# Kernel tuning notes

Measured on AMD Instinct MI355X. Metric: run time of the kernel, lower is better.

Reference implementation:

```python
import jax, jax.numpy as jnp
import numpy as np

N = 20000      # nodes
E = 640000     # edges
FIN = 128
FQK = 128
FV = 128
H = 8
FH = FQK // H   # 16
FHV = FV // H   # 16
FTOT = 2 * FQK + FV


def setup_inputs() -> dict:
    key = jax.random.key(0)
    kx, kw, ks, kd, kb = jax.random.split(key, 5)
    x = jax.random.normal(kx, (N, FIN), dtype=jnp.float32)
    # nn.Linear(Fin, Ftot, bias=False): weight [Ftot, Fin]
    W = jax.random.normal(kw, (FTOT, FIN), dtype=jnp.float32) / np.sqrt(FIN)
    # src must be sorted (scatter ops assume grouped-by-src, size src[-1]+1)
    src = jnp.sort(jax.random.randint(ks, (E,), 0, N, dtype=jnp.int64))
    src = src.at[-1].set(N - 1)  # ensure full output size N
    dest = jax.random.randint(kd, (E,), 0, N, dtype=jnp.int64)
    ei = jnp.stack([src, dest])
    batch = jnp.sort(jax.random.randint(kb, (N,), 0, 16, dtype=jnp.int64))
    return {"x": x, "W": W, "batch": batch, "ei": ei}


def reference(x, W, batch, ei):
    src, dest = ei[0], ei[1]
    scaling = float(FH) ** (-0.5)
    proj = x @ W.T                                  # [N, Ftot]
    q, k, v = jnp.split(proj, [FQK, 2 * FQK], axis=-1)
    q = (q * scaling).reshape(-1, H, FH)            # [N, H, Fh]
    k = k.reshape(-1, H, FH)
    v = v.reshape(-1, H, FHV)
    qs, ks, vs = q[src], k[dest], v[dest]           # [E, H, Fh] gathers
    aw = jnp.einsum('ehf,ehf->eh', qs, ks)          # per-edge dot products
    # scatter_softmax: global (not per-segment) max subtraction, as in source
    xm = aw.max(axis=0)                              # [H]
    exp = jnp.exp(aw - xm) + 1e-8                    # [E, H]
    expsum = jax.ops.segment_sum(exp, src, num_segments=N)[src]
    attn = exp / expsum                              # [E, H]
    out = jax.ops.segment_sum(attn[:, :, None] * vs, src, num_segments=N)
    return out.reshape(-1, H * FHV)                  # [N, Fv]
```

## Files before the change

kernel.cpp:

```cpp
#include <hip/hip_runtime.h>

constexpr int FIN = 128;

constexpr float XM0 = 8.0f;

typedef __attribute__((ext_vector_type(8))) short bf8x;
typedef __attribute__((ext_vector_type(4))) float f4x;
typedef _Float16 h2 __attribute__((ext_vector_type(2)));

__device__ inline unsigned short f2bf(float v) {
  unsigned int u = __float_as_uint(v);
  unsigned int r = u + 0x7FFFu + ((u >> 16) & 1u);
  return (unsigned short)(r >> 16);
}
__device__ inline float bf2f(unsigned short s) {
  return __uint_as_float(((unsigned int)s) << 16);
}
__device__ inline unsigned short f2h(float v) {
  _Float16 h = (_Float16)v;
  return __builtin_bit_cast(unsigned short, h);
}
__device__ inline h2 bch2(float f) { return __builtin_bit_cast(h2, f); }
__device__ inline float bcf(h2 h) { return __builtin_bit_cast(float, h); }

__device__ inline float dot2acc(h2 a, h2 b, float c) {
#if __has_builtin(__builtin_amdgcn_fdot2)
  return __builtin_amdgcn_fdot2(a, b, c, false);
#else
  return c + (float)a[0] * (float)b[0] + (float)a[1] * (float)b[1];
#endif
}

__global__ __launch_bounds__(256, 2) void proj_kernel(
    const float* __restrict__ x, const float* __restrict__ W,
    unsigned short* __restrict__ qg, unsigned short* __restrict__ kvg, int N,
    const int* __restrict__ src, const int* __restrict__ dest,
    unsigned short* __restrict__ dest16, int* __restrict__ row_ptr, int E) {
  __shared__ unsigned short xhi[128][72], xlo[128][72];
  __shared__ unsigned short whi[128][72], wlo[128][72];

  const int tid = threadIdx.x;
  const int r0 = blockIdx.y * 128;
  const int c0 = blockIdx.x * 128;

  {
    const int gid = (blockIdx.y * gridDim.x + blockIdx.x) * 256 + tid;
    const int tot = gridDim.x * gridDim.y * 256;
    for (int i = gid; i < E; i += tot) dest16[i] = (unsigned short)dest[i];
    if (gid <= N) {
      int lo = 0, hi = E;
      while (lo < hi) {
        int mid = (lo + hi) >> 1;
        if (src[mid] < gid) lo = mid + 1; else hi = mid;
      }
      row_ptr[gid] = lo;
    }
  }

  const int lane = tid & 63;
  const int w = tid >> 6;
  const int mbase = (w >> 1) * 64;
  const int nbase = (w & 1) * 64;
  const int lr = lane & 15;
  const int q4 = lane >> 4;

  f4x acc[4][4];
#pragma unroll
  for (int mt = 0; mt < 4; ++mt)
#pragma unroll
    for (int nt = 0; nt < 4; ++nt)
#pragma unroll
      for (int k = 0; k < 4; ++k) acc[mt][nt][k] = 0.f;

  for (int p = 0; p < 2; ++p) {
    if (p) __syncthreads();
#pragma unroll
    for (int pass = 0; pass < 8; ++pass) {
      const int idx = tid + pass * 256;
      const int kq = idx & 15, r = idx >> 4;
      float4 xv = make_float4(0.f, 0.f, 0.f, 0.f);
      if (r0 + r < N) xv = *(const float4*)(x + (size_t)(r0 + r) * FIN + p * 64 + kq * 4);
      const float4 wv = *(const float4*)(W + (size_t)(c0 + r) * FIN + p * 64 + kq * 4);
      const float xa[4] = {xv.x, xv.y, xv.z, xv.w};
      const float wa[4] = {wv.x, wv.y, wv.z, wv.w};
      unsigned short xh[4], xl[4], wh[4], wl[4];
#pragma unroll
      for (int i = 0; i < 4; ++i) {
        xh[i] = f2bf(xa[i]); xl[i] = f2bf(xa[i] - bf2f(xh[i]));
        wh[i] = f2bf(wa[i]); wl[i] = f2bf(wa[i] - bf2f(wh[i]));
      }
      *(ushort4*)&xhi[r][kq * 4] = make_ushort4(xh[0], xh[1], xh[2], xh[3]);
      *(ushort4*)&xlo[r][kq * 4] = make_ushort4(xl[0], xl[1], xl[2], xl[3]);
      *(ushort4*)&whi[r][kq * 4] = make_ushort4(wh[0], wh[1], wh[2], wh[3]);
      *(ushort4*)&wlo[r][kq * 4] = make_ushort4(wl[0], wl[1], wl[2], wl[3]);
    }
    __syncthreads();

#pragma unroll
    for (int kit = 0; kit < 2; ++kit) {
      const int ko = kit * 32 + q4 * 8;
      bf8x ah[4], al[4], bh[4], bl[4];
#pragma unroll
      for (int i2 = 0; i2 < 4; ++i2) {
        ah[i2] = *(const bf8x*)&xhi[mbase + i2 * 16 + lr][ko];
        al[i2] = *(const bf8x*)&xlo[mbase + i2 * 16 + lr][ko];
        bh[i2] = *(const bf8x*)&whi[nbase + i2 * 16 + lr][ko];
        bl[i2] = *(const bf8x*)&wlo[nbase + i2 * 16 + lr][ko];
      }
#pragma unroll
      for (int mt = 0; mt < 4; ++mt)
#pragma unroll
        for (int nt = 0; nt < 4; ++nt) {
          acc[mt][nt] = __builtin_amdgcn_mfma_f32_16x16x32_bf16(ah[mt], bh[nt], acc[mt][nt], 0, 0, 0);
          acc[mt][nt] = __builtin_amdgcn_mfma_f32_16x16x32_bf16(ah[mt], bl[nt], acc[mt][nt], 0, 0, 0);
          acc[mt][nt] = __builtin_amdgcn_mfma_f32_16x16x32_bf16(al[mt], bh[nt], acc[mt][nt], 0, 0, 0);
        }
    }
  }

#pragma unroll
  for (int mt = 0; mt < 4; ++mt)
#pragma unroll
    for (int nt = 0; nt < 4; ++nt)
#pragma unroll
      for (int rr = 0; rr < 4; ++rr) {
        const int row = r0 + mbase + mt * 16 + q4 * 4 + rr;
        if (row < N) {
          const int c = c0 + nbase + nt * 16 + lr;
          const float v = acc[mt][nt][rr];
          if (c < 128) {
            const int head = c >> 4, g = head >> 2, hg = head & 3;
            const int seg = hg * 2 + ((c >> 3) & 1), feat = c & 7;
            qg[((size_t)g * N + row) * 64 + seg * 8 + feat] = f2h(v * 0.25f);
          } else if (c < 256) {
            const int cc = c - 128;
            const int head = cc >> 4, g = head >> 2, hg = head & 3;
            const int seg = hg * 2 + ((cc >> 3) & 1), feat = cc & 7;
            kvg[((size_t)g * N + row) * 128 + seg * 8 + feat] = f2h(v);
          } else {
            const int cc = c - 256;
            const int head = cc >> 4, g = head >> 2, hg = head & 3;
            const int seg = hg * 2 + ((cc >> 3) & 1), feat = cc & 7;
            kvg[((size_t)g * N + row) * 128 + 64 + seg * 8 + feat] = f2h(v);
          }
        }
      }
}

__global__ __launch_bounds__(256, 8) void attn_kernel(
    const unsigned short* __restrict__ qg_, const unsigned short* __restrict__ kvg_,
    const unsigned short* __restrict__ dest16, const int* __restrict__ row_ptr,
    float* __restrict__ out, int N) {
  const _Float16* qg = (const _Float16*)qg_;
  const _Float16* kvg = (const _Float16*)kvg_;

  const int lane = threadIdx.x & 63;
  const int wid = __builtin_amdgcn_readfirstlane(threadIdx.x >> 6);
  const int g = blockIdx.x & 1;
  const int n = (blockIdx.x >> 1) * 4 + wid;
  if (n >= N) return;

  const int seg = lane & 7;
  const int slot = lane >> 3;

  const int e0 = row_ptr[n], e1 = row_ptr[n + 1];

  h2 q2[4];
  {
    const float4 qv = *(const float4*)(qg + ((size_t)g * N + n) * 64 + seg * 8);
    q2[0] = bch2(qv.x); q2[1] = bch2(qv.y); q2[2] = bch2(qv.z); q2[3] = bch2(qv.w);
  }

  const _Float16* kvb = kvg + (size_t)g * N * 128;
  h2 acc4[4] = {h2{0, 0}, h2{0, 0}, h2{0, 0}, h2{0, 0}};
  float es = 0.f;

  for (int cb = e0; cb < e1; cb += 64) {
    const int ee = cb + lane;
    const int dv = dest16[(ee < e1) ? ee : (e1 - 1)];

    const int rem = e1 - cb;
    const int nch = (rem < 64) ? ((rem + 7) >> 3) : 8;

    auto ldkv = [&](int j, float4& kk, float4& vv) {
      const int sl = j * 8 + slot;
      const int d = __shfl(dv, sl);
      const _Float16* kp = kvb + (size_t)d * 128 + seg * 8;
      kk = *(const float4*)kp;
      vv = *(const float4*)(kp + 64);
    };

    auto comp = [&](int j, const float4& kk, const float4& vv) {
      float p = 0.f;
      p = dot2acc(q2[0], bch2(kk.x), p);
      p = dot2acc(q2[1], bch2(kk.y), p);
      p = dot2acc(q2[2], bch2(kk.z), p);
      p = dot2acc(q2[3], bch2(kk.w), p);
      const float s = p + __shfl_xor(p, 1);
      const int e = cb + j * 8 + slot;
      const float a = (e < e1) ? (__expf(s - XM0) + 1e-8f) : 0.f;
      es += a;
      const _Float16 a1 = (_Float16)a;
      const h2 av = {a1, a1};
      acc4[0] = __builtin_elementwise_fma(av, bch2(vv.x), acc4[0]);
      acc4[1] = __builtin_elementwise_fma(av, bch2(vv.y), acc4[1]);
      acc4[2] = __builtin_elementwise_fma(av, bch2(vv.z), acc4[2]);
      acc4[3] = __builtin_elementwise_fma(av, bch2(vv.w), acc4[3]);
    };

    float4 kkA, vvA, kkB, vvB;
    ldkv(0, kkA, vvA);
    ldkv(1, kkB, vvB);

    for (int j = 0; j < nch; j += 2) {
      float4 kkA2, vvA2, kkB2, vvB2;
      const bool pf = (j + 2 < nch);
      if (pf) { ldkv(j + 2, kkA2, vvA2); ldkv(j + 3, kkB2, vvB2); }
      comp(j, kkA, vvA);
      comp(j + 1, kkB, vvB);
      if (pf) { kkA = kkA2; vvA = vvA2; kkB = kkB2; vvB = vvB2; }
    }
  }

#pragma unroll
  for (int st = 8; st <= 32; st <<= 1) {
#pragma unroll
    for (int j = 0; j < 4; ++j) {
      const h2 o = bch2(__shfl_xor(bcf(acc4[j]), st));
      acc4[j] = acc4[j] + o;
    }
    es += __shfl_xor(es, st);
  }

  if (slot == 0) {
    const float inv = (e1 > e0) ? (1.0f / es) : 0.f;
    const int head = g * 4 + (seg >> 1);
    const int half = seg & 1;
    float o[8];
#pragma unroll
    for (int j = 0; j < 4; ++j) {
      o[2 * j] = (float)acc4[j][0] * inv;
      o[2 * j + 1] = (float)acc4[j][1] * inv;
    }
    float* op = out + (size_t)n * 128 + head * 16 + half * 8;
    *(float4*)op = make_float4(o[0], o[1], o[2], o[3]);
    *(float4*)(op + 4) = make_float4(o[4], o[5], o[6], o[7]);
  }
}

extern "C" void kernel_launch(void* const* d_in, const int* in_sizes, int n_in,
                              void* d_out, int out_size, void* d_ws, size_t ws_size,
                              hipStream_t stream) {
  const float* x = (const float*)d_in[0];
  const float* W = (const float*)d_in[1];
  const int* ei = (const int*)d_in[3];

  const int N = in_sizes[0] / FIN;
  const int E = in_sizes[3] / 2;
  const int* src = ei;
  const int* dst = ei + E;
  float* out = (float*)d_out;

  char* ws = (char*)d_ws;
  unsigned short* qg = (unsigned short*)ws;
  size_t off = (size_t)2 * N * 64 * sizeof(unsigned short);
  unsigned short* kvg = (unsigned short*)(ws + off);
  off += (size_t)2 * N * 128 * sizeof(unsigned short);
  unsigned short* dest16 = (unsigned short*)(ws + off);
  off += ((size_t)E * sizeof(unsigned short) + 15) & ~15ull;
  int* row_ptr = (int*)(ws + off);

  dim3 pgrid(3, (N + 127) / 128);
  proj_kernel<<<pgrid, 256, 0, stream>>>(x, W, qg, kvg, N, src, dst, dest16, row_ptr, E);
  attn_kernel<<<((N + 3) / 4) * 2, 256, 0, stream>>>(qg, kvg, dest16, row_ptr, out, N);
}
```

Baseline: 115.7 us.

## Process two nodes per wavefront by splitting lanes into half-wave groups

The attention kernel now gives each 64-lane wavefront two destination nodes, one per 32-lane half, with 4 edge slots per half instead of 8 for one node. Edge chunks shrink to 32, and the loop runs while either half still has edges. The cross-slot reduction drops one shuffle stage and the grid is halved. The goal is to cut per-wave fixed overhead and reduction cost on low-degree nodes. The cost is that each wave now loops until the busier of its two nodes is done, so imbalance between paired nodes wastes lanes.

```diff
diff --git a/kernel.cpp b/kernel.cpp
--- a/kernel.cpp
+++ b/kernel.cpp
@@ -157,11 +157,13 @@
   const int lane = threadIdx.x & 63;
   const int wid = __builtin_amdgcn_readfirstlane(threadIdx.x >> 6);
   const int g = blockIdx.x & 1;
-  const int n = (blockIdx.x >> 1) * 4 + wid;
-  if (n >= N) return;
-
+  const int n0 = (blockIdx.x >> 1) * 8 + wid * 2;
+  if (n0 >= N) return;
+
+  const int nh = lane >> 5;
+  const int slot = (lane >> 3) & 3;
   const int seg = lane & 7;
-  const int slot = lane >> 3;
+  const int n = n0 + nh;
 
   const int e0 = row_ptr[n], e1 = row_ptr[n + 1];
 
@@ -175,16 +177,20 @@
   h2 acc4[4] = {h2{0, 0}, h2{0, 0}, h2{0, 0}, h2{0, 0}};
   float es = 0.f;
 
-  for (int cb = e0; cb < e1; cb += 64) {
-    const int ee = cb + lane;
-    const int dv = dest16[(ee < e1) ? ee : (e1 - 1)];
-
-    const int rem = e1 - cb;
-    const int nch = (rem < 64) ? ((rem + 7) >> 3) : 8;
+  int cb = e0;
+  int rem = e1 - e0;
+  while (__any(rem > 0)) {
+    const int l32 = lane & 31;
+    const int dv = dest16[(l32 < rem) ? (cb + l32) : 0];
+
+    const int rem_o = __shfl_xor(rem, 32);
+    int mrem = (rem > rem_o) ? rem : rem_o;
+    if (mrem > 32) mrem = 32;
+    if (mrem < 1) mrem = 1;
+    const int nch = (mrem + 3) >> 2;
 
     auto ldkv = [&](int j, float4& kk, float4& vv) {
-      const int sl = j * 8 + slot;
-      const int d = __shfl(dv, sl);
+      const int d = __shfl(dv, (lane & 32) + j * 4 + slot);
       const _Float16* kp = kvb + (size_t)d * 128 + seg * 8;
       kk = *(const float4*)kp;
       vv = *(const float4*)(kp + 64);
@@ -197,8 +203,7 @@
       p = dot2acc(q2[2], bch2(kk.z), p);
       p = dot2acc(q2[3], bch2(kk.w), p);
       const float s = p + __shfl_xor(p, 1);
-      const int e = cb + j * 8 + slot;
-      const float a = (e < e1) ? (__expf(s - XM0) + 1e-8f) : 0.f;
+      const float a = (j * 4 + slot < rem) ? (__expf(s - XM0) + 1e-8f) : 0.f;
       es += a;
       const _Float16 a1 = (_Float16)a;
       const h2 av = {a1, a1};
@@ -220,10 +225,14 @@
       comp(j + 1, kkB, vvB);
       if (pf) { kkA = kkA2; vvA = vvA2; kkB = kkB2; vvB = vvB2; }
     }
-  }
-
-#pragma unroll
-  for (int st = 8; st <= 32; st <<= 1) {
+
+    cb += 32;
+    rem -= 32;
+    if (rem < 0) rem = 0;
+  }
+
+#pragma unroll
+  for (int st = 8; st <= 16; st <<= 1) {
 #pragma unroll
     for (int j = 0; j < 4; ++j) {
       const h2 o = bch2(__shfl_xor(bcf(acc4[j]), st));
@@ -235,14 +244,14 @@
   if (slot == 0) {
     const float inv = (e1 > e0) ? (1.0f / es) : 0.f;
     const int head = g * 4 + (seg >> 1);
-    const int half = seg & 1;
+    const int halfF = seg & 1;
     float o[8];
 #pragma unroll
     for (int j = 0; j < 4; ++j) {
       o[2 * j] = (float)acc4[j][0] * inv;
       o[2 * j + 1] = (float)acc4[j][1] * inv;
     }
-    float* op = out + (size_t)n * 128 + head * 16 + half * 8;
+    float* op = out + (size_t)n * 128 + head * 16 + halfF * 8;
     *(float4*)op = make_float4(o[0], o[1], o[2], o[3]);
     *(float4*)(op + 4) = make_float4(o[4], o[5], o[6], o[7]);
   }
@@ -272,5 +281,5 @@
 
   dim3 pgrid(3, (N + 127) / 128);
   proj_kernel<<<pgrid, 256, 0, stream>>>(x, W, qg, kvg, N, src, dst, dest16, row_ptr, E);
-  attn_kernel<<<((N + 3) / 4) * 2, 256, 0, stream>>>(qg, kvg, dest16, row_ptr, out, N);
-}
+  attn_kernel<<<((N + 7) / 8) * 2, 256, 0, stream>>>(qg, kvg, dest16, row_ptr, out, N);
+}
```

New measurement: 152.8 us. +32.1%, slower.
